# Optimization experiments

Measured on AMD Instinct MI355X. Metric: run time of the kernel, lower is better.

## Reference

```python
import jax, jax.numpy as jnp
import numpy as np

N = 100000
E = 1600000
IN_C = 128
HID = 128
OUT_C = 2
EPS = 1e-5


def gcn_conv(x, src, dst, norm, W, b, num_nodes):
    # PyG GCNConv: linear transform then symmetric-normalized scatter-add
    h = x @ W                                  # [N, out]
    msg = h[src] * norm[:, None]               # [E+N, out] gather
    out = jax.ops.segment_sum(msg, dst, num_segments=num_nodes)
    return out + b


def batchnorm_eval(x, gamma, beta, rm, rv):
    inv = gamma / jnp.sqrt(rv + EPS)
    return (x - rm) * inv + beta


def setup_inputs() -> dict:
    key = jax.random.key(0)
    ks = jax.random.split(key, 16)
    x = jax.random.normal(ks[0], (N, IN_C), dtype=jnp.float32)
    edge_index = jax.random.randint(ks[1], (2, E), 0, N, dtype=jnp.int32)
    s = 1.0 / np.sqrt(IN_C)
    W1 = jax.random.uniform(ks[2], (IN_C, HID), jnp.float32, -s, s)
    b1 = jnp.zeros((HID,), jnp.float32)
    g1 = jnp.ones((HID,), jnp.float32)
    be1 = jnp.zeros((HID,), jnp.float32)
    rm1 = jax.random.normal(ks[3], (HID,), jnp.float32) * 0.1
    rv1 = jax.random.uniform(ks[4], (HID,), jnp.float32, 0.5, 1.5)
    s2 = 1.0 / np.sqrt(HID)
    W2 = jax.random.uniform(ks[5], (HID, HID), jnp.float32, -s2, s2)
    b2 = jnp.zeros((HID,), jnp.float32)
    g2 = jnp.ones((HID,), jnp.float32)
    be2 = jnp.zeros((HID,), jnp.float32)
    rm2 = jax.random.normal(ks[6], (HID,), jnp.float32) * 0.1
    rv2 = jax.random.uniform(ks[7], (HID,), jnp.float32, 0.5, 1.5)
    W3 = jax.random.uniform(ks[8], (HID, OUT_C), jnp.float32, -s2, s2)
    b3 = jnp.zeros((OUT_C,), jnp.float32)
    return {"x": x, "edge_index": edge_index,
            "W1": W1, "b1": b1, "g1": g1, "be1": be1, "rm1": rm1, "rv1": rv1,
            "W2": W2, "b2": b2, "g2": g2, "be2": be2, "rm2": rm2, "rv2": rv2,
            "W3": W3, "b3": b3}


def reference(x, edge_index, W1, b1, g1, be1, rm1, rv1,
              W2, b2, g2, be2, rm2, rv2, W3, b3):
    num_nodes = x.shape[0]
    loops = jnp.arange(num_nodes, dtype=edge_index.dtype)
    src = jnp.concatenate([edge_index[0], loops])   # add self loops
    dst = jnp.concatenate([edge_index[1], loops])
    deg = jax.ops.segment_sum(jnp.ones_like(dst, dtype=x.dtype), dst,
                              num_segments=num_nodes)
    dinv = jax.lax.rsqrt(deg)                        # deg >= 1 with self loops
    norm = dinv[src] * dinv[dst]                     # [E+N]

    h = gcn_conv(x, src, dst, norm, W1, b1, num_nodes)
    h = jax.nn.relu(batchnorm_eval(h, g1, be1, rm1, rv1))
    h = gcn_conv(h, src, dst, norm, W2, b2, num_nodes)
    h = jax.nn.relu(batchnorm_eval(h, g2, be2, rm2, rv2))
    out = gcn_conv(h, src, dst, norm, W3, b3, num_nodes)
    return out
```

## Files before the change

### kernel.cpp

```cpp
#include <hip/hip_runtime.h>

#define NN 100000
#define EE 1600000
#define CH 128

typedef _Float16 h2 __attribute__((ext_vector_type(2)));
typedef _Float16 h8 __attribute__((ext_vector_type(8)));
typedef float f32x4 __attribute__((ext_vector_type(4)));

#define S_NODES 512
#define NBUCK 196
#define CAP_E 10240


__global__ __launch_bounds__(256) void k_passA(const int* __restrict__ src, const int* __restrict__ dst,
                                               int* __restrict__ gcur, int* __restrict__ eb) {
    __shared__ int hist[NBUCK];
    __shared__ int curL[NBUCK];
    for (int t = threadIdx.x; t < NBUCK; t += 256) hist[t] = 0;
    __syncthreads();
    int base = blockIdx.x * 4096;
    int pk[16], bk[16];
#pragma unroll
    for (int j = 0; j < 16; ++j) {
        int i = base + threadIdx.x + 256 * j;
        if (i < EE) {
            int s = src[i], d = dst[i];
            bk[j] = d >> 9;
            pk[j] = (s << 9) | (d & 511);
            atomicAdd(&hist[bk[j]], 1);
        } else bk[j] = -1;
    }
    __syncthreads();
    for (int t = threadIdx.x; t < NBUCK; t += 256) {
        int h = hist[t];
        curL[t] = (h > 0) ? atomicAdd(&gcur[t], h) : 0;
    }
    __syncthreads();
#pragma unroll
    for (int j = 0; j < 16; ++j) {
        if (bk[j] >= 0) {
            int pos = atomicAdd(&curL[bk[j]], 1);
            if (pos < CAP_E) eb[bk[j] * CAP_E + pos] = pk[j];
        }
    }
}


__global__ __launch_bounds__(256) void k_bscan(const int* __restrict__ gcur, int* __restrict__ bbase,
                                               int* __restrict__ rp) {
    __shared__ int ts[256];
    int t = threadIdx.x;
    int nn = (t < NBUCK) ? min(S_NODES, NN - t * S_NODES) : 0;
    int v = (t < NBUCK) ? (min(gcur[t], CAP_E) + nn) : 0;
    ts[t] = v; __syncthreads();
    for (int off = 1; off < 256; off <<= 1) {
        int u = (t >= off) ? ts[t - off] : 0;
        __syncthreads();
        ts[t] += u;
        __syncthreads();
    }
    if (t < NBUCK) bbase[t] = ts[t] - v;
    if (t == 0) rp[NN] = EE + NN;
}


__global__ __launch_bounds__(256) void k_passB(const int* __restrict__ gcur, const int* __restrict__ eb,
                                               const int* __restrict__ bbase, int* __restrict__ rp,
                                               float* __restrict__ dinv, int* __restrict__ col) {
    __shared__ int c[S_NODES];
    __shared__ int excl[S_NODES];
    __shared__ int cur[S_NODES];
    __shared__ int ts[256];
    __shared__ int stage[CAP_E + S_NODES];
    int bId = blockIdx.x;
    int nbase = bId * S_NODES;
    int tid = threadIdx.x;
    c[tid] = 0; c[tid + 256] = 0;
    __syncthreads();
    int n = min(gcur[bId], CAP_E);
    const int* e = eb + (size_t)bId * CAP_E;
    for (int i = tid; i < n; i += 256) atomicAdd(&c[e[i] & 511], 1);
    __syncthreads();
    int n0 = nbase + 2 * tid, n1 = n0 + 1;
    int v0 = (n0 < NN) ? c[2 * tid] + 1 : 0;
    int v1 = (n1 < NN) ? c[2 * tid + 1] + 1 : 0;
    int s = v0 + v1;
    ts[tid] = s; __syncthreads();
    for (int off = 1; off < 256; off <<= 1) {
        int u = (tid >= off) ? ts[tid - off] : 0;
        __syncthreads();
        ts[tid] += u;
        __syncthreads();
    }
    int ex = ts[tid] - s;
    int base = bbase[bId];
    excl[2 * tid] = ex; excl[2 * tid + 1] = ex + v0;
    cur[2 * tid] = ex;  cur[2 * tid + 1] = ex + v0;
    if (n0 < NN) { rp[n0] = base + ex;      dinv[n0] = rsqrtf((float)v0); }
    if (n1 < NN) { rp[n1] = base + ex + v0; dinv[n1] = rsqrtf((float)v1); }
    __syncthreads();
    for (int i = tid; i < n; i += 256) {
        int pe = e[i];
        int pos = atomicAdd(&cur[pe & 511], 1);
        stage[pos] = pe >> 9;
    }
    {
        int t0 = 2 * tid, t1 = 2 * tid + 1;
        if (n0 < NN) stage[excl[t0] + c[t0]] = n0;
        if (n1 < NN) stage[excl[t1] + c[t1]] = n1;
    }
    __syncthreads();
    int total = ts[255];
    for (int i = tid; i < total; i += 256) col[base + i] = stage[i];
}


__global__ __launch_bounds__(128) void k_prep(const float* __restrict__ W1, const float* __restrict__ W2,
                                              _Float16* __restrict__ Wt1, _Float16* __restrict__ Wt2,
                                              const float* __restrict__ b1, const float* __restrict__ g1,
                                              const float* __restrict__ be1, const float* __restrict__ rm1,
                                              const float* __restrict__ rv1,
                                              const float* __restrict__ b2, const float* __restrict__ g2,
                                              const float* __restrict__ be2, const float* __restrict__ rm2,
                                              const float* __restrict__ rv2,
                                              float* __restrict__ sc1, float* __restrict__ sh1,
                                              float* __restrict__ sc2, float* __restrict__ sh2) {
    int bid = blockIdx.x, t = threadIdx.x;
    if (bid < 128) {
        Wt1[bid * 128 + t] = (_Float16)W1[t * 128 + bid];
    } else if (bid < 256) {
        int nn = bid - 128;
        Wt2[nn * 128 + t] = (_Float16)W2[t * 128 + nn];
    } else if (bid == 256) {
        float sv = g1[t] * rsqrtf(rv1[t] + 1e-5f);
        sc1[t] = sv;
        sh1[t] = (b1[t] - rm1[t]) * sv + be1[t];
    } else {
        float sv = g2[t] * rsqrtf(rv2[t] + 1e-5f);
        sc2[t] = sv;
        sh2[t] = (b2[t] - rm2[t]) * sv + be2[t];
    }
}


template <bool F32IN>
__global__ __launch_bounds__(256) void k_gemm_mfma(const void* __restrict__ Ain,
                                                   const _Float16* __restrict__ Wt,
                                                   const float* __restrict__ dinv,
                                                   _Float16* __restrict__ C) {
    __shared__ _Float16 Wl[CH * CH];
    {
        const float4* wg = (const float4*)Wt;
#pragma unroll
        for (int i = 0; i < 8; ++i) {
            int chunk = i * 256 + threadIdx.x;
            int row = chunk >> 4, slot = chunk & 15;
            float4 v = wg[chunk];
            *(float4*)((char*)Wl + row * 256 + ((slot ^ (row & 15)) * 16)) = v;
        }
    }
    __syncthreads();
    int lane = threadIdx.x & 63;
    int l15 = lane & 15, lhi = lane >> 4;
    int row0 = blockIdx.x * 64 + (threadIdx.x >> 6) * 16;
    if (row0 >= NN) return;

    h8 afrag[4];
    if (F32IN) {
        const float* Arow = (const float*)Ain + (size_t)(row0 + l15) * CH + lhi * 8;
#pragma unroll
        for (int ks = 0; ks < 4; ++ks) {
            float4 a = *(const float4*)(Arow + ks * 32);
            float4 b = *(const float4*)(Arow + ks * 32 + 4);
            h8 o;
            o[0] = (_Float16)a.x; o[1] = (_Float16)a.y; o[2] = (_Float16)a.z; o[3] = (_Float16)a.w;
            o[4] = (_Float16)b.x; o[5] = (_Float16)b.y; o[6] = (_Float16)b.z; o[7] = (_Float16)b.w;
            afrag[ks] = o;
        }
    } else {
        const _Float16* Arow = (const _Float16*)Ain + (size_t)(row0 + l15) * CH + lhi * 8;
#pragma unroll
        for (int ks = 0; ks < 4; ++ks) afrag[ks] = *(const h8*)(Arow + ks * 32);
    }

    f32x4 acc[8] = {};
#pragma unroll
    for (int ks = 0; ks < 4; ++ks) {
        int slot = ks * 4 + lhi;
#pragma unroll
        for (int c = 0; c < 8; ++c) {
            int brow = c * 16 + l15;
            h8 b = *(const h8*)((char*)Wl + brow * 256 + ((slot ^ (brow & 15)) * 16));
            acc[c] = __builtin_amdgcn_mfma_f32_16x16x32_f16(afrag[ks], b, acc[c], 0, 0, 0);
        }
    }
    float dv[4];
#pragma unroll
    for (int j = 0; j < 4; ++j) dv[j] = dinv[row0 + lhi * 4 + j];
#pragma unroll
    for (int c = 0; c < 8; ++c)
#pragma unroll
        for (int j = 0; j < 4; ++j) {
            float v = acc[c][j] * dv[j];
            C[(size_t)(row0 + lhi * 4 + j) * CH + c * 16 + l15] = (_Float16)v;
        }
}


__global__ __launch_bounds__(256) void k_agg128h(const _Float16* __restrict__ h, const int* __restrict__ rp,
                                                 const int* __restrict__ col, const float* __restrict__ dinv,
                                                 const float* __restrict__ sc, const float* __restrict__ sh,
                                                 _Float16* __restrict__ out) {
    int node = blockIdx.x * 4 + (threadIdx.x >> 6);
    if (node >= NN) return;
    node = __builtin_amdgcn_readfirstlane(node);
    int lane = threadIdx.x & 63;
    int beg = rp[node], end = rp[node + 1];
    float ax = 0.f, ay = 0.f;
    int e = beg;
    for (; e + 8 <= end; e += 8) {
        int s0 = col[e], s1 = col[e + 1], s2 = col[e + 2], s3 = col[e + 3];
        int s4 = col[e + 4], s5 = col[e + 5], s6 = col[e + 6], s7 = col[e + 7];
        h2 v0 = *(const h2*)(h + (size_t)s0 * CH + lane * 2);
        h2 v1 = *(const h2*)(h + (size_t)s1 * CH + lane * 2);
        h2 v2 = *(const h2*)(h + (size_t)s2 * CH + lane * 2);
        h2 v3 = *(const h2*)(h + (size_t)s3 * CH + lane * 2);
        h2 v4 = *(const h2*)(h + (size_t)s4 * CH + lane * 2);
        h2 v5 = *(const h2*)(h + (size_t)s5 * CH + lane * 2);
        h2 v6 = *(const h2*)(h + (size_t)s6 * CH + lane * 2);
        h2 v7 = *(const h2*)(h + (size_t)s7 * CH + lane * 2);
        ax += ((float)v0[0] + (float)v1[0]) + ((float)v2[0] + (float)v3[0])
            + ((float)v4[0] + (float)v5[0]) + ((float)v6[0] + (float)v7[0]);
        ay += ((float)v0[1] + (float)v1[1]) + ((float)v2[1] + (float)v3[1])
            + ((float)v4[1] + (float)v5[1]) + ((float)v6[1] + (float)v7[1]);
    }
    if (e + 4 <= end) {
        int s0 = col[e], s1 = col[e + 1], s2 = col[e + 2], s3 = col[e + 3];
        h2 v0 = *(const h2*)(h + (size_t)s0 * CH + lane * 2);
        h2 v1 = *(const h2*)(h + (size_t)s1 * CH + lane * 2);
        h2 v2 = *(const h2*)(h + (size_t)s2 * CH + lane * 2);
        h2 v3 = *(const h2*)(h + (size_t)s3 * CH + lane * 2);
        ax += ((float)v0[0] + (float)v1[0]) + ((float)v2[0] + (float)v3[0]);
        ay += ((float)v0[1] + (float)v1[1]) + ((float)v2[1] + (float)v3[1]);
        e += 4;
    }
    for (; e < end; ++e) {
        int s0 = col[e];
        h2 v0 = *(const h2*)(h + (size_t)s0 * CH + lane * 2);
        ax += (float)v0[0];
        ay += (float)v0[1];
    }
    float dvn = dinv[node];
    int c = lane * 2;
    float2 scv = *(const float2*)(sc + c);
    float2 shv = *(const float2*)(sh + c);
    float o0 = fmaxf(fmaf(ax * dvn, scv.x, shv.x), 0.f);
    float o1 = fmaxf(fmaf(ay * dvn, scv.y, shv.y), 0.f);
    h2 o; o[0] = (_Float16)o0; o[1] = (_Float16)o1;
    *(h2*)(out + (size_t)node * CH + c) = o;
}


__global__ __launch_bounds__(256) void k_gemm_out(const _Float16* __restrict__ A, const float* __restrict__ W3,
                                                  const float* __restrict__ dinv, float* __restrict__ H3) {
    __shared__ float w3s[256];
    w3s[threadIdx.x] = W3[threadIdx.x];
    __syncthreads();
    int n = blockIdx.x * 256 + threadIdx.x;
    if (n >= NN) return;
    const h8* ar = (const h8*)(A + (size_t)n * CH);
    float a0 = 0.f, a1 = 0.f;
#pragma unroll
    for (int kb = 0; kb < 16; ++kb) {
        h8 a = ar[kb];
#pragma unroll
        for (int j = 0; j < 8; ++j) {
            float av = (float)a[j];
            int k = kb * 8 + j;
            a0 += av * w3s[k * 2];
            a1 += av * w3s[k * 2 + 1];
        }
    }
    float dv = dinv[n];
    *(float2*)(H3 + (size_t)n * 2) = make_float2(a0 * dv, a1 * dv);
}

__global__ __launch_bounds__(256) void k_agg_out(const float* __restrict__ H3, const int* __restrict__ rp,
                                                 const int* __restrict__ col, const float* __restrict__ dinv,
                                                 const float* __restrict__ b3, float* __restrict__ out) {
    int n = blockIdx.x * 256 + threadIdx.x;
    if (n >= NN) return;
    int beg = rp[n], end = rp[n + 1];
    float a0 = 0.f, a1 = 0.f;
    for (int e = beg; e < end; ++e) {
        int s = col[e];
        float2 hv = *(const float2*)(H3 + (size_t)s * 2);
        a0 += hv.x;
        a1 += hv.y;
    }
    float dv = dinv[n];
    out[(size_t)n * 2 + 0] = fmaf(a0, dv, b3[0]);
    out[(size_t)n * 2 + 1] = fmaf(a1, dv, b3[1]);
}


extern "C" void kernel_launch(void* const* d_in, const int* in_sizes, int n_in,
                              void* d_out, int out_size, void* d_ws, size_t ws_size,
                              hipStream_t stream) {
    const float* x  = (const float*)d_in[0];
    const int* ei   = (const int*)d_in[1];
    const int* src  = ei;
    const int* dst  = ei + EE;
    const float* W1 = (const float*)d_in[2];
    const float* b1 = (const float*)d_in[3];
    const float* g1 = (const float*)d_in[4];
    const float* be1 = (const float*)d_in[5];
    const float* rm1 = (const float*)d_in[6];
    const float* rv1 = (const float*)d_in[7];
    const float* W2 = (const float*)d_in[8];
    const float* b2 = (const float*)d_in[9];
    const float* g2 = (const float*)d_in[10];
    const float* be2 = (const float*)d_in[11];
    const float* rm2 = (const float*)d_in[12];
    const float* rv2 = (const float*)d_in[13];
    const float* W3 = (const float*)d_in[14];
    const float* b3 = (const float*)d_in[15];
    float* out = (float*)d_out;

    char* p = (char*)d_ws;
    auto carve = [&](size_t bytes) -> void* {
        void* r = (void*)p;
        p += (bytes + 255) & ~(size_t)255;
        return r;
    };
    int* rp     = (int*)carve((size_t)(NN + 1) * 4);
    float* dinv = (float*)carve((size_t)NN * 4);
    int* col    = (int*)carve((size_t)(EE + NN) * 4);
    int* bbase  = (int*)carve(256 * 4);
    float* sc1  = (float*)carve(128 * 4);
    float* sh1  = (float*)carve(128 * 4);
    float* sc2  = (float*)carve(128 * 4);
    float* sh2  = (float*)carve(128 * 4);
    _Float16* bufA = (_Float16*)carve((size_t)NN * CH * 2);
    _Float16* bufB = (_Float16*)carve((size_t)NN * CH * 2);
    _Float16* Wt1  = (_Float16*)carve(128 * 128 * 2);
    _Float16* Wt2  = (_Float16*)carve(128 * 128 * 2);
    float* h3   = (float*)carve((size_t)NN * 2 * 4);

    int* eb   = (int*)bufA;
    int* gcur = eb + (size_t)NBUCK * CAP_E;

    hipMemsetAsync(gcur, 0, (size_t)NBUCK * 4, stream);

    k_passA<<<(EE + 4095) / 4096, 256, 0, stream>>>(src, dst, gcur, eb);
    k_bscan<<<1, 256, 0, stream>>>(gcur, bbase, rp);
    k_passB<<<NBUCK, 256, 0, stream>>>(gcur, eb, bbase, rp, dinv, col);
    k_prep<<<258, 128, 0, stream>>>(W1, W2, Wt1, Wt2,
                                    b1, g1, be1, rm1, rv1,
                                    b2, g2, be2, rm2, rv2,
                                    sc1, sh1, sc2, sh2);

    k_gemm_mfma<true><<<(NN + 63) / 64, 256, 0, stream>>>(x, Wt1, dinv, bufA);
    k_agg128h<<<(NN + 3) / 4, 256, 0, stream>>>(bufA, rp, col, dinv, sc1, sh1, bufB);
    k_gemm_mfma<false><<<(NN + 63) / 64, 256, 0, stream>>>(bufB, Wt2, dinv, bufA);
    k_agg128h<<<(NN + 3) / 4, 256, 0, stream>>>(bufA, rp, col, dinv, sc2, sh2, bufB);
    k_gemm_out<<<(NN + 255) / 256, 256, 0, stream>>>(bufB, W3, dinv, h3);
    k_agg_out<<<(NN + 255) / 256, 256, 0, stream>>>(h3, rp, col, dinv, b3, out);
}
```

Measured before the change: 228.0 us.

## Store hidden features in channel-chunked layout and aggregate one chunk per block

Changes the intermediate feature layout from row-major [N,128] to eight 16-channel chunks of [N,16], written by the MFMA GEMM and read by the next GEMM and the output GEMM. The aggregation kernel now assigns each block a single channel chunk (blockIdx & 7) and 16 nodes per wave, with 8 lanes per edge, 8 edges in flight per wave, and a shuffle reduction. The aim is a smaller gather working set per pass, since each chunk is 3.2 MB, which should improve cache hit rates on random neighbor gathers. In exchange, each 32-byte gathered row is much smaller than a cache line, the column indices are re-read eight times, and there are extra shuffles and tail predication.

```diff
diff --git a/kernel.cpp b/kernel.cpp
--- a/kernel.cpp
+++ b/kernel.cpp
@@ -11,6 +11,8 @@
 #define S_NODES 512
 #define NBUCK 196
 #define CAP_E 10240
+
+#define CHUNK_STRIDE ((size_t)NN * 16)
 
 
 __global__ __launch_bounds__(256) void k_passA(const int* __restrict__ src, const int* __restrict__ dst,
@@ -179,9 +181,13 @@
             afrag[ks] = o;
         }
     } else {
-        const _Float16* Arow = (const _Float16*)Ain + (size_t)(row0 + l15) * CH + lhi * 8;
-#pragma unroll
-        for (int ks = 0; ks < 4; ++ks) afrag[ks] = *(const h8*)(Arow + ks * 32);
+        const _Float16* Ah = (const _Float16*)Ain;
+#pragma unroll
+        for (int ks = 0; ks < 4; ++ks) {
+            int chunk = ks * 2 + (lhi >> 1);
+            afrag[ks] = *(const h8*)(Ah + (size_t)chunk * CHUNK_STRIDE
+                                     + (size_t)(row0 + l15) * 16 + (lhi & 1) * 8);
+        }
     }
 
     f32x4 acc[8] = {};
@@ -203,62 +209,62 @@
 #pragma unroll
         for (int j = 0; j < 4; ++j) {
             float v = acc[c][j] * dv[j];
-            C[(size_t)(row0 + lhi * 4 + j) * CH + c * 16 + l15] = (_Float16)v;
-        }
-}
-
-
-__global__ __launch_bounds__(256) void k_agg128h(const _Float16* __restrict__ h, const int* __restrict__ rp,
-                                                 const int* __restrict__ col, const float* __restrict__ dinv,
-                                                 const float* __restrict__ sc, const float* __restrict__ sh,
-                                                 _Float16* __restrict__ out) {
-    int node = blockIdx.x * 4 + (threadIdx.x >> 6);
-    if (node >= NN) return;
-    node = __builtin_amdgcn_readfirstlane(node);
+            C[(size_t)c * CHUNK_STRIDE + (size_t)(row0 + lhi * 4 + j) * 16 + l15] = (_Float16)v;
+        }
+}
+
+
+#define NPW 16
+
+__global__ __launch_bounds__(256) void k_aggs(const _Float16* __restrict__ h, const int* __restrict__ rp,
+                                              const int* __restrict__ col, const float* __restrict__ dinv,
+                                              const float* __restrict__ sc, const float* __restrict__ sh,
+                                              _Float16* __restrict__ out) {
+    int s = blockIdx.x & 7;
+    int g = blockIdx.x >> 3;
     int lane = threadIdx.x & 63;
-    int beg = rp[node], end = rp[node + 1];
-    float ax = 0.f, ay = 0.f;
-    int e = beg;
-    for (; e + 8 <= end; e += 8) {
-        int s0 = col[e], s1 = col[e + 1], s2 = col[e + 2], s3 = col[e + 3];
-        int s4 = col[e + 4], s5 = col[e + 5], s6 = col[e + 6], s7 = col[e + 7];
-        h2 v0 = *(const h2*)(h + (size_t)s0 * CH + lane * 2);
-        h2 v1 = *(const h2*)(h + (size_t)s1 * CH + lane * 2);
-        h2 v2 = *(const h2*)(h + (size_t)s2 * CH + lane * 2);
-        h2 v3 = *(const h2*)(h + (size_t)s3 * CH + lane * 2);
-        h2 v4 = *(const h2*)(h + (size_t)s4 * CH + lane * 2);
-        h2 v5 = *(const h2*)(h + (size_t)s5 * CH + lane * 2);
-        h2 v6 = *(const h2*)(h + (size_t)s6 * CH + lane * 2);
-        h2 v7 = *(const h2*)(h + (size_t)s7 * CH + lane * 2);
-        ax += ((float)v0[0] + (float)v1[0]) + ((float)v2[0] + (float)v3[0])
-            + ((float)v4[0] + (float)v5[0]) + ((float)v6[0] + (float)v7[0]);
-        ay += ((float)v0[1] + (float)v1[1]) + ((float)v2[1] + (float)v3[1])
-            + ((float)v4[1] + (float)v5[1]) + ((float)v6[1] + (float)v7[1]);
-    }
-    if (e + 4 <= end) {
-        int s0 = col[e], s1 = col[e + 1], s2 = col[e + 2], s3 = col[e + 3];
-        h2 v0 = *(const h2*)(h + (size_t)s0 * CH + lane * 2);
-        h2 v1 = *(const h2*)(h + (size_t)s1 * CH + lane * 2);
-        h2 v2 = *(const h2*)(h + (size_t)s2 * CH + lane * 2);
-        h2 v3 = *(const h2*)(h + (size_t)s3 * CH + lane * 2);
-        ax += ((float)v0[0] + (float)v1[0]) + ((float)v2[0] + (float)v3[0]);
-        ay += ((float)v0[1] + (float)v1[1]) + ((float)v2[1] + (float)v3[1]);
-        e += 4;
-    }
-    for (; e < end; ++e) {
-        int s0 = col[e];
-        h2 v0 = *(const h2*)(h + (size_t)s0 * CH + lane * 2);
-        ax += (float)v0[0];
-        ay += (float)v0[1];
-    }
-    float dvn = dinv[node];
-    int c = lane * 2;
-    float2 scv = *(const float2*)(sc + c);
-    float2 shv = *(const float2*)(sh + c);
-    float o0 = fmaxf(fmaf(ax * dvn, scv.x, shv.x), 0.f);
-    float o1 = fmaxf(fmaf(ay * dvn, scv.y, shv.y), 0.f);
-    h2 o; o[0] = (_Float16)o0; o[1] = (_Float16)o1;
-    *(h2*)(out + (size_t)node * CH + c) = o;
+    int grp = lane >> 3, ch8 = lane & 7;
+    const _Float16* hs = h + (size_t)s * CHUNK_STRIDE;
+    _Float16* os = out + (size_t)s * CHUNK_STRIDE;
+    float2 scv = *(const float2*)(sc + s * 16 + ch8 * 2);
+    float2 shv = *(const float2*)(sh + s * 16 + ch8 * 2);
+    int node0 = (g * 4 + (threadIdx.x >> 6)) * NPW;
+    for (int ni = 0; ni < NPW; ++ni) {
+        int node = node0 + ni;
+        if (node >= NN) return;
+        int beg = rp[node], end = rp[node + 1];
+        int lastc = end - 1;
+        int i0 = beg + grp;
+        int i1 = i0 + 8, i2 = i0 + 16, i3 = i0 + 24;
+        int s0 = col[i0 < end ? i0 : lastc];
+        int s1 = col[i1 < end ? i1 : lastc];
+        int s2 = col[i2 < end ? i2 : lastc];
+        int s3 = col[i3 < end ? i3 : lastc];
+        h2 v0 = *(const h2*)(hs + (size_t)s0 * 16 + ch8 * 2);
+        h2 v1 = *(const h2*)(hs + (size_t)s1 * 16 + ch8 * 2);
+        h2 v2 = *(const h2*)(hs + (size_t)s2 * 16 + ch8 * 2);
+        h2 v3 = *(const h2*)(hs + (size_t)s3 * 16 + ch8 * 2);
+        float ax = (i0 < end ? (float)v0[0] : 0.f) + (i1 < end ? (float)v1[0] : 0.f)
+                 + (i2 < end ? (float)v2[0] : 0.f) + (i3 < end ? (float)v3[0] : 0.f);
+        float ay = (i0 < end ? (float)v0[1] : 0.f) + (i1 < end ? (float)v1[1] : 0.f)
+                 + (i2 < end ? (float)v2[1] : 0.f) + (i3 < end ? (float)v3[1] : 0.f);
+        for (int e = beg + 32; e < end; e += 8) {
+            int idx = e + grp;
+            int sr = col[idx < end ? idx : lastc];
+            h2 v = *(const h2*)(hs + (size_t)sr * 16 + ch8 * 2);
+            if (idx < end) { ax += (float)v[0]; ay += (float)v[1]; }
+        }
+        ax += __shfl_xor(ax, 8);  ay += __shfl_xor(ay, 8);
+        ax += __shfl_xor(ax, 16); ay += __shfl_xor(ay, 16);
+        ax += __shfl_xor(ax, 32); ay += __shfl_xor(ay, 32);
+        if (grp == 0) {
+            float dvn = dinv[node];
+            float o0 = fmaxf(fmaf(ax * dvn, scv.x, shv.x), 0.f);
+            float o1 = fmaxf(fmaf(ay * dvn, scv.y, shv.y), 0.f);
+            h2 o; o[0] = (_Float16)o0; o[1] = (_Float16)o1;
+            *(h2*)(os + (size_t)node * 16 + ch8 * 2) = o;
+        }
+    }
 }
 
 
@@ -269,17 +275,22 @@
     __syncthreads();
     int n = blockIdx.x * 256 + threadIdx.x;
     if (n >= NN) return;
-    const h8* ar = (const h8*)(A + (size_t)n * CH);
     float a0 = 0.f, a1 = 0.f;
 #pragma unroll
-    for (int kb = 0; kb < 16; ++kb) {
-        h8 a = ar[kb];
+    for (int c = 0; c < 8; ++c) {
+        h8 a = *(const h8*)(A + (size_t)c * CHUNK_STRIDE + (size_t)n * 16);
+        h8 b = *(const h8*)(A + (size_t)c * CHUNK_STRIDE + (size_t)n * 16 + 8);
 #pragma unroll
         for (int j = 0; j < 8; ++j) {
-            float av = (float)a[j];
-            int k = kb * 8 + j;
-            a0 += av * w3s[k * 2];
-            a1 += av * w3s[k * 2 + 1];
+            int k = c * 16 + j;
+            a0 += (float)a[j] * w3s[k * 2];
+            a1 += (float)a[j] * w3s[k * 2 + 1];
+        }
+#pragma unroll
+        for (int j = 0; j < 8; ++j) {
+            int k = c * 16 + 8 + j;
+            a0 += (float)b[j] * w3s[k * 2];
+            a1 += (float)b[j] * w3s[k * 2 + 1];
         }
     }
     float dv = dinv[n];
@@ -361,10 +372,11 @@
                                     b2, g2, be2, rm2, rv2,
                                     sc1, sh1, sc2, sh2);
 
+    int aggBlocks = 8 * ((NN + 4 * NPW - 1) / (4 * NPW));
     k_gemm_mfma<true><<<(NN + 63) / 64, 256, 0, stream>>>(x, Wt1, dinv, bufA);
-    k_agg128h<<<(NN + 3) / 4, 256, 0, stream>>>(bufA, rp, col, dinv, sc1, sh1, bufB);
+    k_aggs<<<aggBlocks, 256, 0, stream>>>(bufA, rp, col, dinv, sc1, sh1, bufB);
     k_gemm_mfma<false><<<(NN + 63) / 64, 256, 0, stream>>>(bufB, Wt2, dinv, bufA);
-    k_agg128h<<<(NN + 3) / 4, 256, 0, stream>>>(bufA, rp, col, dinv, sc2, sh2, bufB);
+    k_aggs<<<aggBlocks, 256, 0, stream>>>(bufA, rp, col, dinv, sc2, sh2, bufB);
     k_gemm_out<<<(NN + 255) / 256, 256, 0, stream>>>(bufB, W3, dinv, h3);
     k_agg_out<<<(NN + 255) / 256, 256, 0, stream>>>(h3, rp, col, dinv, b3, out);
 }
```

After: 423.3 us. +85.7%, slower.
